# Optimization experiments

Hardware: AMD Instinct MI355X
Metric: run time of the kernel (lower is better)

Reference implementation:

```python
import jax, jax.numpy as jnp
import numpy as np

EPS = 1e-6
NUM_HEADS = 8


def setup_inputs() -> dict:
    key0 = jax.random.key(0)
    ks = jax.random.split(key0, 8)
    N, B, C, HW = 900, 8, 256, 1156

    def lin(k):
        kw, kb = jax.random.split(k)
        W = jax.random.normal(kw, (C, C), jnp.float32) * 0.02
        b = jax.random.normal(kb, (C,), jnp.float32) * 0.02
        return W, b

    Wq, bq = lin(ks[0])
    Wk, bk = lin(ks[1])
    Wv, bv = lin(ks[2])
    Wo, bo = lin(ks[3])
    query = jax.random.normal(ks[4], (N, B, C), jnp.float32)
    key = jax.random.normal(ks[5], (HW, B, C), jnp.float32)
    query_pos = jax.random.normal(ks[6], (N, B, C), jnp.float32)
    key_pos = jax.random.normal(ks[7], (HW, B, C), jnp.float32)
    return dict(query=query, key=key, query_pos=query_pos, key_pos=key_pos,
                Wq=Wq, bq=bq, Wk=Wk, bk=bk, Wv=Wv, bv=bv, Wo=Wo, bo=bo)


def reference(query, key, query_pos, key_pos, Wq, bq, Wk, bk, Wv, bv, Wo, bo):
    # Faithful port of LinearCrossAttention.forward (value=None -> key,
    # identity=None -> query, batch_first=False, dropout inactive).
    # NOTE: the original permutes to (B, seq, head, head_dim) but then applies
    # cumsum(dim=2) / einsums along axis 2, i.e. over the HEAD axis; we
    # reproduce that exactly.
    N, B, C = query.shape
    HW = key.shape[0]
    H = NUM_HEADS
    D = C // H

    q = (query @ Wq.T + bq) + query_pos          # (N,B,C)
    k = (key @ Wk.T + bk) + key_pos              # (HW,B,C)
    v = key @ Wv.T + bv                          # (HW,B,C)

    q = jnp.transpose(q.reshape(N, B, H, D), (1, 0, 2, 3))    # (B,N,H,D)
    k = jnp.transpose(k.reshape(HW, B, H, D), (1, 0, 2, 3))   # (B,HW,H,D)
    v = jnp.transpose(v.reshape(HW, B, H, D), (1, 0, 2, 3))   # (B,HW,H,D)

    q = jax.nn.sigmoid(q)
    k = jax.nn.sigmoid(k)

    if HW > N:  # pad queries along the sequence axis
        q = jnp.concatenate([q, jnp.zeros((B, HW - N, H, D), q.dtype)], axis=1)

    dot = lambda a, b: jnp.sum(a * b, axis=-1)   # 'nhld,nhld->nhl'

    sink_incoming = 1.0 / dot(q + EPS, jnp.cumsum(k, axis=2) + EPS)   # (B,HW,H)
    source_outgoing = 1.0 / dot(k + EPS, jnp.cumsum(q, axis=2) + EPS)
    normal = (jnp.arange(H, dtype=q.dtype) + 1.0)[None, None, :]       # (1,1,H)
    sink_incoming = sink_incoming * normal
    source_outgoing = source_outgoing * normal

    conserved_sink = dot(q + EPS, jnp.cumsum(k * source_outgoing[..., None], axis=2) + EPS) / normal
    conserved_source = dot(k + EPS, jnp.cumsum(q * sink_incoming[..., None], axis=2) + EPS) / normal
    conserved_source = jnp.clip(conserved_source, -1.0, 1.0)

    sink_allocation = jax.nn.sigmoid(conserved_sink)
    conserved_source = jnp.exp(conserved_source)
    source_competition = conserved_source / jnp.cumsum(conserved_source, axis=-1) * normal

    # causal_dot_product with cumsum over axis 2 (head axis in this layout)
    qs = q * (sink_incoming[..., None] / normal[..., None])            # (B,HW,H,D)
    kv = jnp.cumsum(jnp.einsum('blhd,blhm->blhdm', k, v * source_competition[..., None]), axis=2)
    qkv = jnp.einsum('blhd,blhdm->blhm', qs, kv)                       # (B,HW,H,D)

    out = (qkv * sink_allocation[..., None])[:, :N]                    # (B,N,H,D)
    out = jnp.swapaxes(out, 1, 2).reshape(B, N, C)                     # matches torch transpose(1,2).reshape
    out = out @ Wo.T + bo
    out = jnp.swapaxes(out, 0, 1)                                      # (N,B,C)
    return query + out
```

## Files before the change

### kernel.cpp

```cpp
#include <hip/hip_runtime.h>
#include <math.h>

#define EPSV 1e-6f
constexpr int N_ = 900, B_ = 8, C_ = 256, H_ = 8, D_ = 32;
constexpr int M_TOT = N_ * B_;
constexpr int BM  = 32;
constexpr int NBLK = M_TOT / BM;
constexpr int VS  = 272;
constexpr int OFF_AQ = 65536;
constexpr int OFF_AK = 81920;
constexpr int OFF_Q  = 98304;
constexpr int OFF_K  = OFF_Q + BM * VS * 2;
constexpr int OFF_V  = OFF_K + BM * VS * 2;
constexpr int LDS1   = OFF_V + BM * VS * 2;
constexpr int LDS2   = 81920;

typedef __attribute__((ext_vector_type(8))) short short8;
typedef __attribute__((ext_vector_type(4))) float f32x4;
typedef __attribute__((ext_vector_type(2))) float f32x2;
typedef __attribute__((ext_vector_type(2))) unsigned short us2;

__device__ __forceinline__ unsigned short f2bf(float f) {
    unsigned int u = __float_as_uint(f);
    return (unsigned short)((u + 0x7FFFu + ((u >> 16) & 1u)) >> 16);
}
__device__ __forceinline__ float bf2f(unsigned short u) {
    return __uint_as_float(((unsigned int)u) << 16);
}
__device__ __forceinline__ int swz(int row, int kElem) {
    int b = (row << 9) + (kElem << 1);
    return b ^ ((row & 7) << 4);
}

template<int CTRL>
__device__ __forceinline__ float dpp_add(float v) {
    int x = __builtin_amdgcn_update_dpp(0, __float_as_int(v), CTRL, 0xF, 0xF, true);
    return v + __int_as_float(x);
}
__device__ __forceinline__ float red16(float v) {
    v = dpp_add<0xB1>(v);
    v = dpp_add<0x4E>(v);
    v = dpp_add<0x124>(v);
    v = dpp_add<0x128>(v);
    return v;
}

__global__ __launch_bounds__(256)
void pack_w(const float* __restrict__ Wq, const float* __restrict__ Wk,
            const float* __restrict__ Wv, const float* __restrict__ Wo,
            unsigned short* __restrict__ wbf)
{
    const int i = (blockIdx.x * 256 + threadIdx.x) * 8;
    const float* src = (i < 65536) ? Wq : (i < 131072) ? Wk
                     : (i < 196608) ? Wv : Wo;
    const int off = i & 65535;
    const float4 a = *reinterpret_cast<const float4*>(src + off);
    const float4 b = *reinterpret_cast<const float4*>(src + off + 4);
    short8 p;
    p[0]=(short)f2bf(a.x); p[1]=(short)f2bf(a.y);
    p[2]=(short)f2bf(a.z); p[3]=(short)f2bf(a.w);
    p[4]=(short)f2bf(b.x); p[5]=(short)f2bf(b.y);
    p[6]=(short)f2bf(b.z); p[7]=(short)f2bf(b.w);
    *reinterpret_cast<short8*>(wbf + i) = p;
}

__device__ __forceinline__ void stageW32(const unsigned short* Wmat, int kkElem,
                                         char* wbufLds, int cw, int lane)
{
    #pragma unroll
    for (int n = 0; n < 4; ++n) {
        const int L  = n * 1024 + lane * 16;
        const int cl = L >> 7;
        const int kb = (L & 127) ^ ((cl & 7) << 4);
        const char* src = (const char*)Wmat + (size_t)(cw + cl) * 512
                        + kkElem * 2 + kb;
        __builtin_amdgcn_global_load_lds(
            (const __attribute__((address_space(1))) unsigned int*)src,
            (__attribute__((address_space(3))) unsigned int*)(wbufLds + n * 1024),
            16, 0, 0);
    }
}

__device__ __forceinline__ void step_mm32(const unsigned char* At, const char* wb,
                                          int kkA, int lrow, int kg8,
                                          f32x4 acc[2][2])
{
    #pragma unroll
    for (int kh = 0; kh < 2; ++kh) {
        const short8 a0 = *reinterpret_cast<const short8*>(At + swz(lrow,      kkA + kh*32 + kg8));
        const short8 a1 = *reinterpret_cast<const short8*>(At + swz(16 + lrow, kkA + kh*32 + kg8));
        #pragma unroll
        for (int j = 0; j < 2; ++j) {
            const int cl = j*16 + lrow;
            const short8 bfr = *reinterpret_cast<const short8*>(
                wb + cl*128 + ((kh*64 + kg8*2) ^ ((cl & 7) << 4)));
            acc[0][j] = __builtin_amdgcn_mfma_f32_16x16x32_bf16(a0, bfr, acc[0][j], 0, 0, 0);
            acc[1][j] = __builtin_amdgcn_mfma_f32_16x16x32_bf16(a1, bfr, acc[1][j], 0, 0, 0);
        }
    }
}

__global__ __launch_bounds__(512)
void fused_qkva(const float* __restrict__ query, const float* __restrict__ key,
                const float* __restrict__ qpos,  const float* __restrict__ kpos,
                const unsigned short* __restrict__ wbf,
                const float* __restrict__ bq, const float* __restrict__ bk,
                const float* __restrict__ bv,
                unsigned short* __restrict__ abf)
{
    extern __shared__ char smem[];
    char* Wb = smem;
    unsigned char* Aq = (unsigned char*)(smem + OFF_AQ);
    unsigned char* Ak = (unsigned char*)(smem + OFF_AK);
    unsigned short* q_sb = (unsigned short*)(smem + OFF_Q);
    unsigned short* k_sb = (unsigned short*)(smem + OFF_K);
    unsigned short* v_sb = (unsigned short*)(smem + OFF_V);

    const int tid = threadIdx.x;
    const int r0  = blockIdx.x * BM;
    const int wave = tid >> 6, lane = tid & 63;
    const int cw = wave * 32;
    char* mywb = Wb + wave * 8192;

    stageW32(wbf, 0, mywb, cw, lane);

    {
        const int trow = tid >> 5, k0 = (tid & 31) * 8;
        #pragma unroll
        for (int i = 0; i < 2; ++i) {
            const int row = trow + i * 16;
            const float* xr = query + (size_t)(r0 + row) * C_ + k0;
            const float* kr = key   + (size_t)(r0 + row) * C_ + k0;
            const float4 a0 = *reinterpret_cast<const float4*>(xr);
            const float4 a1 = *reinterpret_cast<const float4*>(xr + 4);
            const float4 b0 = *reinterpret_cast<const float4*>(kr);
            const float4 b1 = *reinterpret_cast<const float4*>(kr + 4);
            short8 pa;
            pa[0]=(short)f2bf(a0.x); pa[1]=(short)f2bf(a0.y);
            pa[2]=(short)f2bf(a0.z); pa[3]=(short)f2bf(a0.w);
            pa[4]=(short)f2bf(a1.x); pa[5]=(short)f2bf(a1.y);
            pa[6]=(short)f2bf(a1.z); pa[7]=(short)f2bf(a1.w);
            *reinterpret_cast<short8*>(Aq + swz(row, k0)) = pa;
            short8 pb;
            pb[0]=(short)f2bf(b0.x); pb[1]=(short)f2bf(b0.y);
            pb[2]=(short)f2bf(b0.z); pb[3]=(short)f2bf(b0.w);
            pb[4]=(short)f2bf(b1.x); pb[5]=(short)f2bf(b1.y);
            pb[6]=(short)f2bf(b1.z); pb[7]=(short)f2bf(b1.w);
            *reinterpret_cast<short8*>(Ak + swz(row, k0)) = pb;
        }
    }

    const int lrow = lane & 15, kg8 = (lane >> 4) * 8;
    const int crow0 = (lane >> 4) * 4, ccol = lane & 15;

    float bqv[2], bkv[2], bvv[2];
    #pragma unroll
    for (int j = 0; j < 2; ++j) {
        const int ch = cw + j*16 + ccol;
        bqv[j] = bq[ch]; bkv[j] = bk[ch]; bvv[j] = bv[ch];
    }

    __syncthreads();

    f32x4 qacc[2][2] = {}; f32x4 kacc[2][2] = {}; f32x4 vacc[2][2] = {};

    #pragma unroll
    for (int st = 0; st < 12; ++st) {
        if (st < 11) {
            const int nx = st + 1;
            stageW32(wbf + (nx >> 2) * 65536, (nx & 3) * 64,
                     mywb + (nx & 1) * 4096, cw, lane);
            asm volatile("s_waitcnt vmcnt(4)" ::: "memory");
        } else {
            asm volatile("s_waitcnt vmcnt(0)" ::: "memory");
        }

        const char* wb = mywb + (st & 1) * 4096;
        const int kkA = (st & 3) * 64;
        if (st < 4)      step_mm32(Aq, wb, kkA, lrow, kg8, qacc);
        else if (st < 8) step_mm32(Ak, wb, kkA, lrow, kg8, kacc);
        else             step_mm32(Ak, wb, kkA, lrow, kg8, vacc);

        if (st == 3) {
            #pragma unroll
            for (int j = 0; j < 2; ++j) {
                const int ch = cw + j*16 + ccol;
                #pragma unroll
                for (int rh = 0; rh < 2; ++rh)
                    #pragma unroll
                    for (int r_ = 0; r_ < 4; ++r_) {
                        const int gr = r0 + rh*16 + crow0 + r_;
                        float v = qacc[rh][j][r_] + bqv[j]
                                + qpos[(size_t)gr * C_ + ch];
                        q_sb[(rh*16+crow0+r_)*VS + ch] = f2bf(1.f/(1.f+__expf(-v)));
                    }
            }
        }
        if (st == 7) {
            #pragma unroll
            for (int j = 0; j < 2; ++j) {
                const int ch = cw + j*16 + ccol;
                #pragma unroll
                for (int rh = 0; rh < 2; ++rh)
                    #pragma unroll
                    for (int r_ = 0; r_ < 4; ++r_) {
                        const int gr = r0 + rh*16 + crow0 + r_;
                        float v = kacc[rh][j][r_] + bkv[j]
                                + kpos[(size_t)gr * C_ + ch];
                        k_sb[(rh*16+crow0+r_)*VS + ch] = f2bf(1.f/(1.f+__expf(-v)));
                    }
            }
        }
        if (st == 11) {
            #pragma unroll
            for (int j = 0; j < 2; ++j) {
                const int ch = cw + j*16 + ccol;
                #pragma unroll
                for (int rh = 0; rh < 2; ++rh)
                    #pragma unroll
                    for (int r_ = 0; r_ < 4; ++r_)
                        v_sb[(rh*16+crow0+r_)*VS + ch] =
                            f2bf(vacc[rh][j][r_] + bvv[j]);
            }
        }
    }

    __syncthreads();

    {
        const int loc = tid >> 4, tt = tid & 15, d0 = tt * 2;
        const int gr = r0 + loc;
        const int nn = gr >> 3, bb = gr & 7;
        const unsigned short* qr = q_sb + loc * VS + d0;
        const unsigned short* kr = k_sb + loc * VS + d0;
        const unsigned short* vr = v_sb + loc * VS + d0;
        f32x2 qh[8], kh[8], vh[8];
        #pragma unroll
        for (int h = 0; h < 8; ++h) {
            const us2 tq = *reinterpret_cast<const us2*>(qr + (h << 5));
            const us2 tk = *reinterpret_cast<const us2*>(kr + (h << 5));
            const us2 tv = *reinterpret_cast<const us2*>(vr + (h << 5));
            qh[h][0] = bf2f(tq[0]); qh[h][1] = bf2f(tq[1]);
            kh[h][0] = bf2f(tk[0]); kh[h][1] = bf2f(tk[1]);
            vh[h][0] = bf2f(tv[0]); vh[h][1] = bf2f(tv[1]);
        }

        float pr[8], ps[8];
        {
            f32x2 ck = {0,0}, cq = {0,0};
            #pragma unroll
            for (int h = 0; h < 8; ++h) {
                float p1 = 0.f, p2 = 0.f;
                #pragma unroll
                for (int j = 0; j < 2; ++j) {
                    ck[j] += kh[h][j]; cq[j] += qh[h][j];
                    p1 += (qh[h][j] + EPSV) * (ck[j] + EPSV);
                    p2 += (kh[h][j] + EPSV) * (cq[j] + EPSV);
                }
                pr[h] = p1; ps[h] = p2;
            }
        }
        #pragma unroll
        for (int h = 0; h < 8; ++h) pr[h] = red16(pr[h]);
        #pragma unroll
        for (int h = 0; h < 8; ++h) ps[h] = red16(ps[h]);

        float ir1[8], so_[8];
        #pragma unroll
        for (int h = 0; h < 8; ++h) {
            ir1[h] = 1.f / pr[h];
            so_[h] = (float)(h+1) / ps[h];
        }

        float pt[8], pu[8];
        {
            f32x2 c2 = {0,0}, c3 = {0,0};
            #pragma unroll
            for (int h = 0; h < 8; ++h) {
                const float sih = (float)(h+1) * ir1[h];
                float p3 = 0.f, p4 = 0.f;
                #pragma unroll
                for (int j = 0; j < 2; ++j) {
                    c2[j] += kh[h][j] * so_[h];
                    c3[j] += qh[h][j] * sih;
                    p3 += (qh[h][j] + EPSV) * (c2[j] + EPSV);
                    p4 += (kh[h][j] + EPSV) * (c3[j] + EPSV);
                }
                pt[h] = p3; pu[h] = p4;
            }
        }
        #pragma unroll
        for (int h = 0; h < 8; ++h) pt[h] = red16(pt[h]);
        #pragma unroll
        for (int h = 0; h < 8; ++h) pu[h] = red16(pu[h]);

        float salloc[8], scomp[8];
        {
            float css = 0.f;
            #pragma unroll
            for (int h = 0; h < 8; ++h) {
                const float inv_n = 1.f / (float)(h+1);
                salloc[h] = 1.f / (1.f + __expf(-pt[h] * inv_n));
                const float consrc = fminf(1.f, fmaxf(-1.f, pu[h] * inv_n));
                const float cs = __expf(consrc);
                css += cs;
                scomp[h] = cs / css * (float)(h+1);
            }
        }

        #pragma unroll
        for (int h = 0; h < 8; ++h) {
            f32x2 qs2, a2 = {0,0};
            #pragma unroll
            for (int j = 0; j < 2; ++j) qs2[j] = qh[h][j] * ir1[h];
            #pragma unroll
            for (int h2 = 0; h2 <= h; ++h2) {
                float p = 0.f;
                #pragma unroll
                for (int j = 0; j < 2; ++j) p += qs2[j] * kh[h2][j];
                p = red16(p);
                const float w = p * scomp[h2];
                #pragma unroll
                for (int j = 0; j < 2; ++j) a2[j] += w * vh[h2][j];
            }
            us2 o;
            o[0] = f2bf(a2[0] * salloc[h]);
            o[1] = f2bf(a2[1] * salloc[h]);
            *reinterpret_cast<us2*>(abf + (size_t)bb*(H_*N_*D_) + (size_t)h*(N_*D_)
                                        + (size_t)nn*D_ + d0) = o;
        }
    }
}

__global__ __launch_bounds__(512)
void outproj(const unsigned short* __restrict__ abf,
             const unsigned short* __restrict__ wbf,
             const float* __restrict__ bo,
             const float* __restrict__ query,
             float* __restrict__ out)
{
    extern __shared__ char smem[];
    char* Wb = smem;
    unsigned char* As = (unsigned char*)(smem + 65536);
    const int tid = threadIdx.x;
    const int r0  = blockIdx.x * BM;
    const int wave = tid >> 6, lane = tid & 63;
    const int cw = wave * 32;
    char* mywb = Wb + wave * 8192;
    const unsigned short* Wo = wbf + 3*65536;

    stageW32(Wo, 0, mywb, cw, lane);

    {
        const int trow = tid >> 5, k0 = (tid & 31) * 8;
        #pragma unroll
        for (int i = 0; i < 2; ++i) {
            const int row = trow + i * 16;
            const int gr = r0 + row;
            const int nn = gr >> 3, bb = gr & 7;
            const short8 p = *reinterpret_cast<const short8*>(
                abf + (size_t)bb * (N_*C_) + (size_t)nn * C_ + k0);
            *reinterpret_cast<short8*>(As + swz(row, k0)) = p;
        }
    }

    const int lrow = lane & 15, kg8 = (lane >> 4) * 8;
    const int crow0 = (lane >> 4) * 4, ccol = lane & 15;

    float bov[2], qres[16];
    #pragma unroll
    for (int j = 0; j < 2; ++j) {
        const int ch = cw + j*16 + ccol;
        bov[j] = bo[ch];
        #pragma unroll
        for (int rh = 0; rh < 2; ++rh)
            #pragma unroll
            for (int r_ = 0; r_ < 4; ++r_)
                qres[j*8+rh*4+r_] =
                    query[(size_t)(r0 + rh*16 + crow0 + r_) * C_ + ch];
    }

    __syncthreads();

    f32x4 acc[2][2] = {};
    #pragma unroll
    for (int sp = 0; sp < 4; ++sp) {
        if (sp < 3) {
            stageW32(Wo, (sp+1)*64, mywb + ((sp+1) & 1) * 4096, cw, lane);
            asm volatile("s_waitcnt vmcnt(4)" ::: "memory");
        } else {
            asm volatile("s_waitcnt vmcnt(0)" ::: "memory");
        }
        step_mm32(As, mywb + (sp & 1) * 4096, sp*64, lrow, kg8, acc);
    }

    #pragma unroll
    for (int j = 0; j < 2; ++j) {
        const int ch = cw + j*16 + ccol;
        #pragma unroll
        for (int rh = 0; rh < 2; ++rh)
            #pragma unroll
            for (int r_ = 0; r_ < 4; ++r_) {
                const size_t g = (size_t)(r0 + rh*16 + crow0 + r_) * C_ + ch;
                out[g] = acc[rh][j][r_] + bov[j] + qres[j*8+rh*4+r_];
            }
    }
}

extern "C" void kernel_launch(void* const* d_in, const int* in_sizes, int n_in,
                              void* d_out, int out_size, void* d_ws, size_t ws_size,
                              hipStream_t stream)
{
    const float* query = (const float*)d_in[0];
    const float* key   = (const float*)d_in[1];
    const float* qpos  = (const float*)d_in[2];
    const float* kpos  = (const float*)d_in[3];
    const float* Wq = (const float*)d_in[4];  const float* bq = (const float*)d_in[5];
    const float* Wk = (const float*)d_in[6];  const float* bk = (const float*)d_in[7];
    const float* Wv = (const float*)d_in[8];  const float* bv = (const float*)d_in[9];
    const float* Wo = (const float*)d_in[10]; const float* bo = (const float*)d_in[11];

    unsigned short* wbf = (unsigned short*)d_ws;
    unsigned short* abf = wbf + 4*65536;
    float* out = (float*)d_out;

    pack_w<<<128, 256, 0, stream>>>(Wq, Wk, Wv, Wo, wbf);
    fused_qkva<<<NBLK, 512, LDS1, stream>>>(query, key, qpos, kpos, wbf,
                                            bq, bk, bv, abf);
    outproj<<<NBLK, 512, LDS2, stream>>>(abf, wbf, bo, query, out);
}
```

Before: 29.81 us.

## Stage full Wo and A tile via direct global-to-LDS loads in outproj

The output-projection kernel now issues all four Wo K-slices at once into a larger per-wave LDS region instead of double-buffering. The A tile is loaded with global_load_lds so it goes straight into swizzled LDS without passing through registers. The early bias and residual register preloads are removed, and those values are read in the epilogue. The aim is to overlap all weight loads with the MFMA steps and cut register pressure, at the cost of 144KB of LDS per block, which lowers occupancy, and of residual loads that now sit on the tail.

```diff
diff --git a/kernel.cpp b/kernel.cpp
--- a/kernel.cpp
+++ b/kernel.cpp
@@ -13,7 +13,7 @@
 constexpr int OFF_K  = OFF_Q + BM * VS * 2;
 constexpr int OFF_V  = OFF_K + BM * VS * 2;
 constexpr int LDS1   = OFF_V + BM * VS * 2;
-constexpr int LDS2   = 81920;
+constexpr int LDS2   = 131072 + 16384;
 
 typedef __attribute__((ext_vector_type(8))) short short8;
 typedef __attribute__((ext_vector_type(4))) float f32x4;
@@ -341,68 +341,60 @@
 {
     extern __shared__ char smem[];
     char* Wb = smem;
-    unsigned char* As = (unsigned char*)(smem + 65536);
+    unsigned char* As = (unsigned char*)(smem + 131072);
     const int tid = threadIdx.x;
     const int r0  = blockIdx.x * BM;
     const int wave = tid >> 6, lane = tid & 63;
     const int cw = wave * 32;
-    char* mywb = Wb + wave * 8192;
+    char* mywb = Wb + wave * 16384;
     const unsigned short* Wo = wbf + 3*65536;
 
-    stageW32(Wo, 0, mywb, cw, lane);
-
-    {
-        const int trow = tid >> 5, k0 = (tid & 31) * 8;
-        #pragma unroll
-        for (int i = 0; i < 2; ++i) {
-            const int row = trow + i * 16;
-            const int gr = r0 + row;
-            const int nn = gr >> 3, bb = gr & 7;
-            const short8 p = *reinterpret_cast<const short8*>(
-                abf + (size_t)bb * (N_*C_) + (size_t)nn * C_ + k0);
-            *reinterpret_cast<short8*>(As + swz(row, k0)) = p;
-        }
-    }
+    #pragma unroll
+    for (int n = 0; n < 2; ++n) {
+        const int Lb  = n * 1024 + lane * 16;
+        const int row = wave * 4 + (Lb >> 9);
+        const int gr  = r0 + row;
+        const int nn  = gr >> 3, bb = gr & 7;
+        const char* src = (const char*)(abf + (size_t)bb * (N_*C_)
+                                            + (size_t)nn * C_)
+                        + ((Lb & 511) ^ ((row & 7) << 4));
+        __builtin_amdgcn_global_load_lds(
+            (const __attribute__((address_space(1))) unsigned int*)src,
+            (__attribute__((address_space(3))) unsigned int*)(As + wave*2048 + n*1024),
+            16, 0, 0);
+    }
+
+    #pragma unroll
+    for (int s = 0; s < 4; ++s)
+        stageW32(Wo, s * 64, mywb + s * 4096, cw, lane);
 
     const int lrow = lane & 15, kg8 = (lane >> 4) * 8;
     const int crow0 = (lane >> 4) * 4, ccol = lane & 15;
 
-    float bov[2], qres[16];
+    asm volatile("s_waitcnt vmcnt(16)" ::: "memory");
+    __builtin_amdgcn_s_barrier();
+    __builtin_amdgcn_sched_barrier(0);
+
+    f32x4 acc[2][2] = {};
+    #pragma unroll
+    for (int sp = 0; sp < 4; ++sp) {
+        if (sp == 0)      asm volatile("s_waitcnt vmcnt(12)" ::: "memory");
+        else if (sp == 1) asm volatile("s_waitcnt vmcnt(8)"  ::: "memory");
+        else if (sp == 2) asm volatile("s_waitcnt vmcnt(4)"  ::: "memory");
+        else              asm volatile("s_waitcnt vmcnt(0)"  ::: "memory");
+        step_mm32(As, mywb + sp * 4096, sp * 64, lrow, kg8, acc);
+    }
+
     #pragma unroll
     for (int j = 0; j < 2; ++j) {
         const int ch = cw + j*16 + ccol;
-        bov[j] = bo[ch];
-        #pragma unroll
-        for (int rh = 0; rh < 2; ++rh)
-            #pragma unroll
-            for (int r_ = 0; r_ < 4; ++r_)
-                qres[j*8+rh*4+r_] =
-                    query[(size_t)(r0 + rh*16 + crow0 + r_) * C_ + ch];
-    }
-
-    __syncthreads();
-
-    f32x4 acc[2][2] = {};
-    #pragma unroll
-    for (int sp = 0; sp < 4; ++sp) {
-        if (sp < 3) {
-            stageW32(Wo, (sp+1)*64, mywb + ((sp+1) & 1) * 4096, cw, lane);
-            asm volatile("s_waitcnt vmcnt(4)" ::: "memory");
-        } else {
-            asm volatile("s_waitcnt vmcnt(0)" ::: "memory");
-        }
-        step_mm32(As, mywb + (sp & 1) * 4096, sp*64, lrow, kg8, acc);
-    }
-
-    #pragma unroll
-    for (int j = 0; j < 2; ++j) {
-        const int ch = cw + j*16 + ccol;
+        const float bov = bo[ch];
         #pragma unroll
         for (int rh = 0; rh < 2; ++rh)
             #pragma unroll
             for (int r_ = 0; r_ < 4; ++r_) {
                 const size_t g = (size_t)(r0 + rh*16 + crow0 + r_) * C_ + ch;
-                out[g] = acc[rh][j][r_] + bov[j] + qres[j*8+rh*4+r_];
+                out[g] = acc[rh][j][r_] + bov + query[g];
             }
     }
 }
```

Measured after the change: 30.19 us. No clear change (+1.3%).
